# Kernel tuning notes

Hardware: AMD Instinct MI355X
Metric: run time of the kernel (lower is better)

## Reference

```python
import jax, jax.numpy as jnp
import numpy as np

D = 1024
H = 16
HD = D // H
FFN = D * 2
EPS = 1e-5


def _layernorm(x, g, b):
    mu = jnp.mean(x, axis=-1, keepdims=True)
    var = jnp.var(x, axis=-1, keepdims=True)
    return (x - mu) * jax.lax.rsqrt(var + EPS) * g + b


def setup_inputs() -> dict:
    key = jax.random.key(0)
    ks = jax.random.split(key, 12)
    s = 1.0 / np.sqrt(D)
    inp = {
        "x": jax.random.normal(ks[0], (2, 2048, D), dtype=jnp.float32),
        "Wq": jax.random.normal(ks[1], (D, D), dtype=jnp.float32) * s,
        "bq": jnp.zeros((D,), jnp.float32),
        "Wk": jax.random.normal(ks[2], (D, D), dtype=jnp.float32) * s,
        "bk": jnp.zeros((D,), jnp.float32),
        "Wv": jax.random.normal(ks[3], (D, D), dtype=jnp.float32) * s,
        "bv": jnp.zeros((D,), jnp.float32),
        "Wo": jax.random.normal(ks[4], (D, D), dtype=jnp.float32) * s,
        "bo": jnp.zeros((D,), jnp.float32),
        "g1": jnp.ones((D,), jnp.float32),
        "b1": jnp.zeros((D,), jnp.float32),
        "W_ff1": jax.random.normal(ks[5], (D, FFN), dtype=jnp.float32) * s,
        "b_ff1": jnp.zeros((FFN,), jnp.float32),
        "W_ff2": jax.random.normal(ks[6], (FFN, D), dtype=jnp.float32) * (1.0 / np.sqrt(FFN)),
        "b_ff2": jnp.zeros((D,), jnp.float32),
        "g2": jnp.ones((D,), jnp.float32),
        "b2": jnp.zeros((D,), jnp.float32),
    }
    return inp


def reference(x, Wq, bq, Wk, bk, Wv, bv, Wo, bo, g1, b1, W_ff1, b_ff1, W_ff2, b_ff2, g2, b2):
    B, S, _ = x.shape
    # QKV projections -> [B, H, S, HD]
    def split_heads(t):
        return t.reshape(B, S, H, HD).transpose(0, 2, 1, 3)
    Q = split_heads(x @ Wq + bq)
    K = split_heads(x @ Wk + bk)
    V = split_heads(x @ Wv + bv)
    scores = jnp.einsum('bhqd,bhkd->bhqk', Q, K) / np.sqrt(HD).astype(np.float32)
    attn = jax.nn.softmax(scores, axis=-1)  # dropout = identity in eval
    ctx = jnp.einsum('bhqk,bhkd->bhqd', attn, V)
    ctx = ctx.transpose(0, 2, 1, 3).reshape(B, S, D)
    x = _layernorm(x + ctx @ Wo + bo, g1, b1)
    h = jax.nn.gelu(x @ W_ff1 + b_ff1, approximate=False)
    x = _layernorm(x + h @ W_ff2 + b_ff2, g2, b2)
    return x
```

## Files before the change

kernel.cpp:

```cpp
#include <hip/hip_runtime.h>

#define SEQ 2048
#define NTOK 4096
#define DM 1024
#define LDQK 3072

typedef __attribute__((ext_vector_type(4))) float f32x4;
typedef __attribute__((ext_vector_type(8))) short short8;
typedef __attribute__((ext_vector_type(4))) short short4v;

__device__ __forceinline__ short f2bf(float f) {
  union { float f; unsigned u; } x; x.f = f;
  unsigned r = x.u + 0x7fffu + ((x.u >> 16) & 1u);
  return (short)(r >> 16);
}

__device__ __forceinline__ float bf2f(short s) {
  union { unsigned u; float f; } x;
  x.u = ((unsigned)(unsigned short)s) << 16;
  return x.f;
}

__device__ __forceinline__ void async_load16(const void* g, void* l) {
  __builtin_amdgcn_global_load_lds(
      (const __attribute__((address_space(1))) void*)g,
      (__attribute__((address_space(3))) void*)l, 16, 0, 0);
}

__global__ void __launch_bounds__(256) prep_all(
    const float* __restrict__ Wq, const float* __restrict__ Wk,
    const float* __restrict__ Wv, const float* __restrict__ Wo,
    const float* __restrict__ Wf1, const float* __restrict__ Wf2,
    const float* __restrict__ x,
    short* __restrict__ Wqkv, short* __restrict__ Wto,
    short* __restrict__ Wtf1, short* __restrict__ Wtf2,
    short* __restrict__ xb) {
  const int z = blockIdx.z;
  const int tx = threadIdx.x, ty = threadIdx.y;
  if (z == 6) {
    int blk = blockIdx.y * 64 + blockIdx.x;
    int i = blk * 256 + ty * 32 + tx;
    f32x4 v = ((const f32x4*)x)[i];
    short4v o;
#pragma unroll
    for (int j = 0; j < 4; ++j) o[j] = f2bf(v[j]);
    ((short4v*)xb)[i] = o;
    return;
  }
  const float* in;
  short* out;
  int K, N;
  switch (z) {
    case 0: in = Wq;  out = Wqkv;               K = 1024; N = 1024; break;
    case 1: in = Wk;  out = Wqkv + 1024 * 1024; K = 1024; N = 1024; break;
    case 2: in = Wv;  out = Wqkv + 2048 * 1024; K = 1024; N = 1024; break;
    case 3: in = Wo;  out = Wto;                K = 1024; N = 1024; break;
    case 4: in = Wf1; out = Wtf1;               K = 1024; N = 2048; break;
    default: in = Wf2; out = Wtf2;              K = 2048; N = 1024; break;
  }
  if (blockIdx.x * 32 >= N || blockIdx.y * 32 >= K) return;
  __shared__ float t[32][33];
  const int n = blockIdx.x * 32 + tx;
#pragma unroll
  for (int i = 0; i < 4; ++i) {
    int k = blockIdx.y * 32 + ty + i * 8;
    t[ty + i * 8][tx] = in[(size_t)k * N + n];
  }
  __syncthreads();
  const int k2 = blockIdx.y * 32 + tx;
#pragma unroll
  for (int i = 0; i < 4; ++i) {
    int n2 = blockIdx.x * 32 + ty + i * 8;
    out[(size_t)n2 * K + k2] = f2bf(t[tx][ty + i * 8]);
  }
}

__global__ void __launch_bounds__(512, 2) gemm_qkv8(
    const short* __restrict__ A, const short* __restrict__ Bt,
    const float* __restrict__ bq, const float* __restrict__ bk,
    const float* __restrict__ bv, short* __restrict__ Cout,
    short* __restrict__ VtOut) {
  __shared__ __align__(16) short As[128 * 64];
  __shared__ __align__(16) short Bs[256 * 64];
  const int tid = threadIdx.x;
  const int w = tid >> 6, lane = tid & 63;
  const int hi = lane >> 4, lo = lane & 15;
  const int bx = blockIdx.x, bm = blockIdx.y;
  const int wr = w >> 2, wc = w & 3;
  f32x4 acc[4][4] = {};

  for (int kt = 0; kt < 16; ++kt) {
#pragma unroll
    for (int i = 0; i < 2; ++i) {
      int c = i * 512 + tid;
      int r = c >> 3, scc = (c & 7) ^ (r & 7);
      async_load16(A + (size_t)(bm * 128 + r) * 1024 + kt * 64 + scc * 8,
                   &As[(i * 8 + w) * 512]);
    }
#pragma unroll
    for (int i = 0; i < 4; ++i) {
      int c = i * 512 + tid;
      int r = c >> 3, scc = (c & 7) ^ (r & 7);
      async_load16(Bt + (size_t)(bx * 256 + r) * 1024 + kt * 64 + scc * 8,
                   &Bs[(i * 8 + w) * 512]);
    }
    __syncthreads();
#pragma unroll
    for (int ks = 0; ks < 2; ++ks) {
      short8 af[4], bf[4];
#pragma unroll
      for (int m = 0; m < 4; ++m) {
        int row = wr * 64 + m * 16 + lo;
        int ch = (ks * 4 + hi) ^ (row & 7);
        af[m] = *(const short8*)(&As[row * 64 + ch * 8]);
      }
#pragma unroll
      for (int n = 0; n < 4; ++n) {
        int row = wc * 64 + n * 16 + lo;
        int ch = (ks * 4 + hi) ^ (row & 7);
        bf[n] = *(const short8*)(&Bs[row * 64 + ch * 8]);
      }
#pragma unroll
      for (int m = 0; m < 4; ++m)
#pragma unroll
        for (int n = 0; n < 4; ++n)
          acc[m][n] = __builtin_amdgcn_mfma_f32_16x16x32_bf16(af[m], bf[n], acc[m][n], 0, 0, 0);
    }
    __syncthreads();
  }
  const int colb = bx * 256 + wc * 64 + lo;
#pragma unroll
  for (int m = 0; m < 4; ++m) {
    int row0 = bm * 128 + wr * 64 + m * 16 + hi * 4;
#pragma unroll
    for (int n = 0; n < 4; ++n) {
      int col = colb + n * 16;
      int r3 = col >> 10;
      const float* bp = (r3 == 0) ? bq : ((r3 == 1) ? bk : bv);
      float bs = bp[col & 1023];
      if (r3 == 2) {
        int vdim = col - 2048;
        int hh = vdim >> 6, dd = vdim & 63;
        int bb = row0 >> 11, ss = row0 & 2047;
        short4v t;
#pragma unroll
        for (int j = 0; j < 4; ++j) t[j] = f2bf(acc[m][n][j] + bs);
        *(short4v*)&VtOut[((size_t)(bb * 16 + hh) * 64 + dd) * SEQ + ss] = t;
      } else {
#pragma unroll
        for (int j = 0; j < 4; ++j)
          Cout[(size_t)(row0 + j) * LDQK + col] = f2bf(acc[m][n][j] + bs);
      }
    }
  }
}

template <int EPI, bool DBUF>
__global__ void __launch_bounds__(256, 2) gemm_bt(
    const short* __restrict__ A, const short* __restrict__ Bt,
    const float* __restrict__ b0, void* __restrict__ Cout,
    int M, int N, int K) {
  __shared__ __align__(16) short As[DBUF ? 2 * 128 * 64 : 128 * 64];
  __shared__ __align__(16) short Bs[DBUF ? 2 * 128 * 64 : 128 * 64];
  const int w = threadIdx.x >> 6, lane = threadIdx.x & 63;
  const int hi = lane >> 4, lo = lane & 15;
  const int bm = blockIdx.y, bn = blockIdx.x;
  const int wr = w >> 1, wc = w & 1;
  f32x4 acc[4][4] = {};
  const int nkt = K >> 6;

  auto stage = [&](int kt, int buf) {
#pragma unroll
    for (int j = 0; j < 4; ++j) {
      int c = (j * 4 + w) * 64 + lane;
      int r = c >> 3;
      int scc = (c & 7) ^ (r & 7);
      async_load16(A + (size_t)(bm * 128 + r) * K + kt * 64 + scc * 8,
                   &As[buf * (128 * 64) + (j * 4 + w) * 512]);
      async_load16(Bt + (size_t)(bn * 128 + r) * K + kt * 64 + scc * 8,
                   &Bs[buf * (128 * 64) + (j * 4 + w) * 512]);
    }
  };

  if (DBUF) {
    stage(0, 0);
    __syncthreads();
  }

  for (int kt = 0; kt < nkt; ++kt) {
    int buf = 0;
    if (DBUF) {
      buf = kt & 1;
      if (kt + 1 < nkt) stage(kt + 1, buf ^ 1);
    } else {
      stage(kt, 0);
      __syncthreads();
    }
#pragma unroll
    for (int ks = 0; ks < 2; ++ks) {
      short8 af[4], bf[4];
#pragma unroll
      for (int m = 0; m < 4; ++m) {
        int row = wr * 64 + m * 16 + lo;
        int ch = (ks * 4 + hi) ^ (row & 7);
        af[m] = *(const short8*)(&As[buf * (128 * 64) + row * 64 + ch * 8]);
      }
#pragma unroll
      for (int n = 0; n < 4; ++n) {
        int row = wc * 64 + n * 16 + lo;
        int ch = (ks * 4 + hi) ^ (row & 7);
        bf[n] = *(const short8*)(&Bs[buf * (128 * 64) + row * 64 + ch * 8]);
      }
#pragma unroll
      for (int m = 0; m < 4; ++m)
#pragma unroll
        for (int n = 0; n < 4; ++n)
          acc[m][n] = __builtin_amdgcn_mfma_f32_16x16x32_bf16(af[m], bf[n], acc[m][n], 0, 0, 0);
    }
    __syncthreads();
  }
  const int colb = bn * 128 + wc * 64 + lo;
#pragma unroll
  for (int m = 0; m < 4; ++m) {
    int row0 = bm * 128 + wr * 64 + m * 16 + hi * 4;
#pragma unroll
    for (int n = 0; n < 4; ++n) {
      int col = colb + n * 16;
      float bs = b0[col];
#pragma unroll
      for (int j = 0; j < 4; ++j) {
        float v = acc[m][n][j] + bs;
        if (EPI == 1) v = 0.5f * v * (1.f + erff(v * 0.70710678f));
        ((short*)Cout)[(size_t)(row0 + j) * N + col] = f2bf(v);
      }
    }
  }
}

__global__ void __launch_bounds__(256, 2) gemm_n64(
    const short* __restrict__ A, const short* __restrict__ Bt,
    const float* __restrict__ b0, const short* __restrict__ resid,
    short* __restrict__ Cout, int M, int N, int K) {
  __shared__ __align__(16) short As[2][128 * 64];
  __shared__ __align__(16) short Bs[2][64 * 64];
  const int w = threadIdx.x >> 6, lane = threadIdx.x & 63;
  const int hi = lane >> 4, lo = lane & 15;
  const int bm = blockIdx.y, bn = blockIdx.x;
  const int wr = w >> 1, wc = w & 1;
  f32x4 acc[4][2] = {};
  const int nkt = K >> 6;

  auto stage = [&](int kt, int buf) {
#pragma unroll
    for (int j = 0; j < 4; ++j) {
      int c = (j * 4 + w) * 64 + lane;
      int r = c >> 3;
      int scc = (c & 7) ^ (r & 7);
      async_load16(A + (size_t)(bm * 128 + r) * K + kt * 64 + scc * 8,
                   &As[buf][(j * 4 + w) * 512]);
    }
#pragma unroll
    for (int j = 0; j < 2; ++j) {
      int c = j * 256 + w * 64 + lane;
      int r = c >> 3;
      int scc = (c & 7) ^ (r & 7);
      async_load16(Bt + (size_t)(bn * 64 + r) * K + kt * 64 + scc * 8,
                   &Bs[buf][(j * 256 + w * 64) * 8]);
    }
  };

  stage(0, 0);
  __syncthreads();

  for (int kt = 0; kt < nkt; ++kt) {
    const int buf = kt & 1;
    if (kt + 1 < nkt) stage(kt + 1, buf ^ 1);
#pragma unroll
    for (int ks = 0; ks < 2; ++ks) {
      short8 af[4], bf[2];
#pragma unroll
      for (int m = 0; m < 4; ++m) {
        int row = wr * 64 + m * 16 + lo;
        int ch = (ks * 4 + hi) ^ (row & 7);
        af[m] = *(const short8*)(&As[buf][row * 64 + ch * 8]);
      }
#pragma unroll
      for (int n = 0; n < 2; ++n) {
        int row = wc * 32 + n * 16 + lo;
        int ch = (ks * 4 + hi) ^ (row & 7);
        bf[n] = *(const short8*)(&Bs[buf][row * 64 + ch * 8]);
      }
#pragma unroll
      for (int m = 0; m < 4; ++m)
#pragma unroll
        for (int n = 0; n < 2; ++n)
          acc[m][n] = __builtin_amdgcn_mfma_f32_16x16x32_bf16(af[m], bf[n], acc[m][n], 0, 0, 0);
    }
    __syncthreads();
  }
  const int colb = bn * 64 + wc * 32 + lo;
#pragma unroll
  for (int m = 0; m < 4; ++m) {
    int row0 = bm * 128 + wr * 64 + m * 16 + hi * 4;
#pragma unroll
    for (int n = 0; n < 2; ++n) {
      int col = colb + n * 16;
      float bs = b0[col];
#pragma unroll
      for (int j = 0; j < 4; ++j) {
        size_t idx = (size_t)(row0 + j) * N + col;
        Cout[idx] = f2bf(acc[m][n][j] + bs + bf2f(resid[idx]));
      }
    }
  }
}

__global__ void __launch_bounds__(256, 2) attn_kernel(
    const short* __restrict__ Qb, const short* __restrict__ Kb,
    const short* __restrict__ Vt, short* __restrict__ ctx) {
  const int w = threadIdx.x >> 6, lane = threadIdx.x & 63;
  const int hi = lane >> 4, lo = lane & 15;
  const int tid = threadIdx.x;
  const int L = blockIdx.x;
  const int W = (L & 7) * 128 + (L >> 3);
  const int qt = W & 31, bh = W >> 5;
  const int b = bh >> 4, h = bh & 15;
  const int qbase = qt * 64 + w * 16;
  const float C = 0.18033688f;

  __shared__ __align__(16) short Ks[2][64 * 64];
  __shared__ __align__(16) short Vs[2][64 * 64];
  __shared__ __align__(16) short P[4][16 * 64];

  const short* qp = Qb + (size_t)(b * SEQ + qbase + lo) * LDQK + h * 64;
  short8 bq[2];
#pragma unroll
  for (int c = 0; c < 2; ++c)
    bq[c] = *(const short8*)(qp + c * 32 + hi * 8);

  const short* kb = Kb + (size_t)(b * SEQ) * LDQK + h * 64;
  const short* vb = Vt + (size_t)bh * 64 * SEQ;

  auto stage = [&](int kt, int buf) {
    const short* kg = kb + (size_t)(kt * 64) * LDQK;
#pragma unroll
    for (int i = 0; i < 2; ++i) {
      int c = i * 256 + tid;
      int r = c >> 3, scc = (c & 7) ^ (r & 7);
      async_load16(kg + (size_t)r * LDQK + scc * 8,
                   &Ks[buf][(i * 256 + w * 64) * 8]);
    }
    const short* vg = vb + kt * 64;
#pragma unroll
    for (int i = 0; i < 2; ++i) {
      int c = i * 256 + tid;
      int r = c >> 3, sc2 = (c & 7) ^ (r & 7);
      async_load16(vg + (size_t)r * SEQ + sc2 * 8,
                   &Vs[buf][(i * 256 + w * 64) * 8]);
    }
  };

  stage(0, 0);
  __syncthreads();

  f32x4 o[4] = {};
  float lacc = 0.f;
  const int x7 = lo & 7;

  for (int kt = 0; kt < SEQ / 64; ++kt) {
    const int buf = kt & 1;
    if (kt + 1 < SEQ / 64) stage(kt + 1, buf ^ 1);

    f32x4 s[4] = {};
    __builtin_amdgcn_s_setprio(1);
#pragma unroll
    for (int g = 0; g < 4; ++g) {
      const short* kr = &Ks[buf][(g * 16 + lo) * 64];
      short8 ka0 = *(const short8*)(kr + ((hi) ^ x7) * 8);
      short8 ka1 = *(const short8*)(kr + ((4 + hi) ^ x7) * 8);
      s[g] = __builtin_amdgcn_mfma_f32_16x16x32_bf16(ka0, bq[0], s[g], 0, 0, 0);
      s[g] = __builtin_amdgcn_mfma_f32_16x16x32_bf16(ka1, bq[1], s[g], 0, 0, 0);
    }
    __builtin_amdgcn_s_setprio(0);
    short8 vv[2][4];
#pragma unroll
    for (int ks = 0; ks < 2; ++ks)
#pragma unroll
      for (int a = 0; a < 4; ++a)
        vv[ks][a] = *(const short8*)(&Vs[buf][(a * 16 + lo) * 64 + (((ks * 4 + hi) ^ x7) * 8)]);

    float rsg[4];
    short* pbase = &P[w][0];
#pragma unroll
    for (int g = 0; g < 4; ++g) {
      float p0 = exp2f(s[g][0] * C);
      float p1 = exp2f(s[g][1] * C);
      float p2 = exp2f(s[g][2] * C);
      float p3 = exp2f(s[g][3] * C);
      rsg[g] = (p0 + p1) + (p2 + p3);
      unsigned w0, w1;
      asm("v_cvt_pk_bf16_f32 %0, %1, %2" : "=v"(w0) : "v"(p0), "v"(p1));
      asm("v_cvt_pk_bf16_f32 %0, %1, %2" : "=v"(w1) : "v"(p2), "v"(p3));
      union { unsigned uu[2]; short4v s4; } cv;
      cv.uu[0] = w0; cv.uu[1] = w1;
      int pc = (2 * g + (hi >> 1)) ^ x7;
      *(short4v*)(pbase + lo * 64 + pc * 8 + (hi & 1) * 4) = cv.s4;
    }
    __builtin_amdgcn_s_setprio(1);
#pragma unroll
    for (int ks = 0; ks < 2; ++ks) {
      int pc = (ks * 4 + hi) ^ x7;
      short8 pa = *(const short8*)(pbase + lo * 64 + pc * 8);
#pragma unroll
      for (int a = 0; a < 4; ++a)
        o[a] = __builtin_amdgcn_mfma_f32_16x16x32_bf16(pa, vv[ks][a], o[a], 0, 0, 0);
    }
    __builtin_amdgcn_s_setprio(0);
    lacc += (rsg[0] + rsg[1]) + (rsg[2] + rsg[3]);
    __syncthreads();
  }
  lacc += __shfl_xor(lacc, 16);
  lacc += __shfl_xor(lacc, 32);
#pragma unroll
  for (int j = 0; j < 4; ++j) {
    float lj = __shfl(lacc, hi * 4 + j);
    float inv = 1.f / lj;
    int row = qbase + hi * 4 + j;
#pragma unroll
    for (int a = 0; a < 4; ++a)
      ctx[(size_t)(b * SEQ + row) * DM + h * 64 + a * 16 + lo] = f2bf(o[a][j] * inv);
  }
}

__global__ void __launch_bounds__(256) ln_bf16(
    const short* __restrict__ in, const float* __restrict__ g,
    const float* __restrict__ beta, float* __restrict__ outf,
    short* __restrict__ outb) {
  const int row = blockIdx.x;
  const int t = threadIdx.x;
  const size_t base = (size_t)row * DM;
  short4v iv = ((const short4v*)(in + base))[t];
  f32x4 v;
#pragma unroll
  for (int j = 0; j < 4; ++j) v[j] = bf2f(iv[j]);
  float s = v[0] + v[1] + v[2] + v[3];
  float s2 = v[0] * v[0] + v[1] * v[1] + v[2] * v[2] + v[3] * v[3];
#pragma unroll
  for (int off = 1; off < 64; off <<= 1) {
    s += __shfl_xor(s, off);
    s2 += __shfl_xor(s2, off);
  }
  __shared__ float rs[4], rs2[4];
  if ((t & 63) == 0) { rs[t >> 6] = s; rs2[t >> 6] = s2; }
  __syncthreads();
  s = rs[0] + rs[1] + rs[2] + rs[3];
  s2 = rs2[0] + rs2[1] + rs2[2] + rs2[3];
  float mu = s * (1.f / DM);
  float var = s2 * (1.f / DM) - mu * mu;
  float rstd = rsqrtf(var + 1e-5f);
  f32x4 gv = ((const f32x4*)g)[t];
  f32x4 bv = ((const f32x4*)beta)[t];
  f32x4 ov;
#pragma unroll
  for (int j = 0; j < 4; ++j) ov[j] = (v[j] - mu) * rstd * gv[j] + bv[j];
  if (outf) ((f32x4*)(outf + base))[t] = ov;
  if (outb) {
    short4v sb;
#pragma unroll
    for (int j = 0; j < 4; ++j) sb[j] = f2bf(ov[j]);
    ((short4v*)(outb + base))[t] = sb;
  }
}

extern "C" void kernel_launch(void* const* d_in, const int* in_sizes, int n_in,
                              void* d_out, int out_size, void* d_ws, size_t ws_size,
                              hipStream_t stream) {
  (void)in_sizes; (void)n_in; (void)out_size; (void)ws_size;
  const float* x   = (const float*)d_in[0];
  const float* Wq  = (const float*)d_in[1];
  const float* bq  = (const float*)d_in[2];
  const float* Wk  = (const float*)d_in[3];
  const float* bk  = (const float*)d_in[4];
  const float* Wv  = (const float*)d_in[5];
  const float* bv  = (const float*)d_in[6];
  const float* Wo  = (const float*)d_in[7];
  const float* bo  = (const float*)d_in[8];
  const float* g1  = (const float*)d_in[9];
  const float* b1  = (const float*)d_in[10];
  const float* Wf1 = (const float*)d_in[11];
  const float* bf1 = (const float*)d_in[12];
  const float* Wf2 = (const float*)d_in[13];
  const float* bf2 = (const float*)d_in[14];
  const float* g2  = (const float*)d_in[15];
  const float* b2  = (const float*)d_in[16];

  char* ws = (char*)d_ws;
  const size_t MB = 1u << 20;
  short* Wqkv = (short*)(ws + 0 * MB);
  short* Wto  = (short*)(ws + 6 * MB);
  short* Wtf1 = (short*)(ws + 8 * MB);
  short* Wtf2 = (short*)(ws + 12 * MB);
  short* xb   = (short*)(ws + 16 * MB);
  short* QKV  = (short*)(ws + 24 * MB);
  short* Vt   = (short*)(ws + 48 * MB);
  short* ctxb = (short*)(ws + 56 * MB);
  short* aout = (short*)(ws + 64 * MB);
  short* x1b  = (short*)(ws + 72 * MB);
  short* hb   = QKV;
  short* ffo  = (short*)(ws + 48 * MB);

  prep_all<<<dim3(64, 64, 7), dim3(32, 8), 0, stream>>>(
      Wq, Wk, Wv, Wo, Wf1, Wf2, x, Wqkv, Wto, Wtf1, Wtf2, xb);

  gemm_qkv8<<<dim3(12, 32), 512, 0, stream>>>(xb, Wqkv, bq, bk, bv, QKV, Vt);

  attn_kernel<<<dim3(1024), 256, 0, stream>>>(QKV, QKV + 1024, Vt, ctxb);

  gemm_n64<<<dim3(16, 32), 256, 0, stream>>>(ctxb, Wto, bo, xb, aout, NTOK, 1024, 1024);
  ln_bf16<<<4096, 256, 0, stream>>>(aout, g1, b1, nullptr, x1b);
  gemm_bt<1, true><<<dim3(16, 32), 256, 0, stream>>>(
      x1b, Wtf1, bf1, hb, NTOK, 2048, 1024);
  gemm_n64<<<dim3(16, 32), 256, 0, stream>>>(hb, Wtf2, bf2, x1b, ffo, NTOK, 1024, 2048);
  ln_bf16<<<4096, 256, 0, stream>>>(ffo, g2, b2, (float*)d_out, nullptr);
}
```

Before: 206.5 us.

## Replace output-proj and FFN GEMMs with unified 8-wave single-buffered kernel

Swaps the double-buffered 4-wave gemm_bt and gemm_n64 kernels for one templated 512-thread, 8-wave kernel used by the output projection and both FFN GEMMs. It uses larger N tiles (128 or 256) with a single LDS buffer. The aim is more waves per CU to hide latency and more reuse per tile, with fewer blocks (256 instead of 512). The cost is that loads no longer overlap compute, since each k-step stages synchronously, and the larger per-block tile may reduce occupancy.

Measured after the change: 217.1 us. 5.1% more time.

```diff
diff --git a/kernel.cpp b/kernel.cpp
--- a/kernel.cpp
+++ b/kernel.cpp
@@ -155,161 +155,76 @@
   }
 }
 
-template <int EPI, bool DBUF>
-__global__ void __launch_bounds__(256, 2) gemm_bt(
+template <int EPI, int BN, bool RESID>
+__global__ void __launch_bounds__(512, 2) gemm_w8(
     const short* __restrict__ A, const short* __restrict__ Bt,
-    const float* __restrict__ b0, void* __restrict__ Cout,
-    int M, int N, int K) {
-  __shared__ __align__(16) short As[DBUF ? 2 * 128 * 64 : 128 * 64];
-  __shared__ __align__(16) short Bs[DBUF ? 2 * 128 * 64 : 128 * 64];
-  const int w = threadIdx.x >> 6, lane = threadIdx.x & 63;
+    const float* __restrict__ b0, const short* __restrict__ resid,
+    short* __restrict__ Cout, int M, int N, int K) {
+  constexpr int FR = BN / 64;
+  __shared__ __align__(16) short As[128 * 64];
+  __shared__ __align__(16) short Bs[BN * 64];
+  const int tid = threadIdx.x;
+  const int w = tid >> 6, lane = tid & 63;
   const int hi = lane >> 4, lo = lane & 15;
-  const int bm = blockIdx.y, bn = blockIdx.x;
-  const int wr = w >> 1, wc = w & 1;
-  f32x4 acc[4][4] = {};
+  const int bx = blockIdx.x, bm = blockIdx.y;
+  const int wr = w >> 2, wc = w & 3;
+  f32x4 acc[4][FR] = {};
   const int nkt = K >> 6;
 
-  auto stage = [&](int kt, int buf) {
-#pragma unroll
-    for (int j = 0; j < 4; ++j) {
-      int c = (j * 4 + w) * 64 + lane;
-      int r = c >> 3;
-      int scc = (c & 7) ^ (r & 7);
+  for (int kt = 0; kt < nkt; ++kt) {
+#pragma unroll
+    for (int i = 0; i < 2; ++i) {
+      int c = i * 512 + tid;
+      int r = c >> 3, scc = (c & 7) ^ (r & 7);
       async_load16(A + (size_t)(bm * 128 + r) * K + kt * 64 + scc * 8,
-                   &As[buf * (128 * 64) + (j * 4 + w) * 512]);
-      async_load16(Bt + (size_t)(bn * 128 + r) * K + kt * 64 + scc * 8,
-                   &Bs[buf * (128 * 64) + (j * 4 + w) * 512]);
-    }
-  };
-
-  if (DBUF) {
-    stage(0, 0);
+                   &As[(i * 8 + w) * 512]);
+    }
+#pragma unroll
+    for (int i = 0; i < BN / 64; ++i) {
+      int c = i * 512 + tid;
+      int r = c >> 3, scc = (c & 7) ^ (r & 7);
+      async_load16(Bt + (size_t)(bx * BN + r) * K + kt * 64 + scc * 8,
+                   &Bs[(i * 8 + w) * 512]);
+    }
     __syncthreads();
-  }
-
-  for (int kt = 0; kt < nkt; ++kt) {
-    int buf = 0;
-    if (DBUF) {
-      buf = kt & 1;
-      if (kt + 1 < nkt) stage(kt + 1, buf ^ 1);
-    } else {
-      stage(kt, 0);
-      __syncthreads();
-    }
 #pragma unroll
     for (int ks = 0; ks < 2; ++ks) {
-      short8 af[4], bf[4];
+      short8 af[4], bf[FR];
 #pragma unroll
       for (int m = 0; m < 4; ++m) {
         int row = wr * 64 + m * 16 + lo;
         int ch = (ks * 4 + hi) ^ (row & 7);
-        af[m] = *(const short8*)(&As[buf * (128 * 64) + row * 64 + ch * 8]);
-      }
-#pragma unroll
-      for (int n = 0; n < 4; ++n) {
-        int row = wc * 64 + n * 16 + lo;
+        af[m] = *(const short8*)(&As[row * 64 + ch * 8]);
+      }
+#pragma unroll
+      for (int n = 0; n < FR; ++n) {
+        int row = wc * (BN / 4) + n * 16 + lo;
         int ch = (ks * 4 + hi) ^ (row & 7);
-        bf[n] = *(const short8*)(&Bs[buf * (128 * 64) + row * 64 + ch * 8]);
+        bf[n] = *(const short8*)(&Bs[row * 64 + ch * 8]);
       }
 #pragma unroll
       for (int m = 0; m < 4; ++m)
 #pragma unroll
-        for (int n = 0; n < 4; ++n)
+        for (int n = 0; n < FR; ++n)
           acc[m][n] = __builtin_amdgcn_mfma_f32_16x16x32_bf16(af[m], bf[n], acc[m][n], 0, 0, 0);
     }
     __syncthreads();
   }
-  const int colb = bn * 128 + wc * 64 + lo;
+  const int colb = bx * BN + wc * (BN / 4) + lo;
 #pragma unroll
   for (int m = 0; m < 4; ++m) {
     int row0 = bm * 128 + wr * 64 + m * 16 + hi * 4;
 #pragma unroll
-    for (int n = 0; n < 4; ++n) {
+    for (int n = 0; n < FR; ++n) {
       int col = colb + n * 16;
       float bs = b0[col];
 #pragma unroll
       for (int j = 0; j < 4; ++j) {
+        size_t idx = (size_t)(row0 + j) * N + col;
         float v = acc[m][n][j] + bs;
         if (EPI == 1) v = 0.5f * v * (1.f + erff(v * 0.70710678f));
-        ((short*)Cout)[(size_t)(row0 + j) * N + col] = f2bf(v);
-      }
-    }
-  }
-}
-
-__global__ void __launch_bounds__(256, 2) gemm_n64(
-    const short* __restrict__ A, const short* __restrict__ Bt,
-    const float* __restrict__ b0, const short* __restrict__ resid,
-    short* __restrict__ Cout, int M, int N, int K) {
-  __shared__ __align__(16) short As[2][128 * 64];
-  __shared__ __align__(16) short Bs[2][64 * 64];
-  const int w = threadIdx.x >> 6, lane = threadIdx.x & 63;
-  const int hi = lane >> 4, lo = lane & 15;
-  const int bm = blockIdx.y, bn = blockIdx.x;
-  const int wr = w >> 1, wc = w & 1;
-  f32x4 acc[4][2] = {};
-  const int nkt = K >> 6;
-
-  auto stage = [&](int kt, int buf) {
-#pragma unroll
-    for (int j = 0; j < 4; ++j) {
-      int c = (j * 4 + w) * 64 + lane;
-      int r = c >> 3;
-      int scc = (c & 7) ^ (r & 7);
-      async_load16(A + (size_t)(bm * 128 + r) * K + kt * 64 + scc * 8,
-                   &As[buf][(j * 4 + w) * 512]);
-    }
-#pragma unroll
-    for (int j = 0; j < 2; ++j) {
-      int c = j * 256 + w * 64 + lane;
-      int r = c >> 3;
-      int scc = (c & 7) ^ (r & 7);
-      async_load16(Bt + (size_t)(bn * 64 + r) * K + kt * 64 + scc * 8,
-                   &Bs[buf][(j * 256 + w * 64) * 8]);
-    }
-  };
-
-  stage(0, 0);
-  __syncthreads();
-
-  for (int kt = 0; kt < nkt; ++kt) {
-    const int buf = kt & 1;
-    if (kt + 1 < nkt) stage(kt + 1, buf ^ 1);
-#pragma unroll
-    for (int ks = 0; ks < 2; ++ks) {
-      short8 af[4], bf[2];
-#pragma unroll
-      for (int m = 0; m < 4; ++m) {
-        int row = wr * 64 + m * 16 + lo;
-        int ch = (ks * 4 + hi) ^ (row & 7);
-        af[m] = *(const short8*)(&As[buf][row * 64 + ch * 8]);
-      }
-#pragma unroll
-      for (int n = 0; n < 2; ++n) {
-        int row = wc * 32 + n * 16 + lo;
-        int ch = (ks * 4 + hi) ^ (row & 7);
-        bf[n] = *(const short8*)(&Bs[buf][row * 64 + ch * 8]);
-      }
-#pragma unroll
-      for (int m = 0; m < 4; ++m)
-#pragma unroll
-        for (int n = 0; n < 2; ++n)
-          acc[m][n] = __builtin_amdgcn_mfma_f32_16x16x32_bf16(af[m], bf[n], acc[m][n], 0, 0, 0);
-    }
-    __syncthreads();
-  }
-  const int colb = bn * 64 + wc * 32 + lo;
-#pragma unroll
-  for (int m = 0; m < 4; ++m) {
-    int row0 = bm * 128 + wr * 64 + m * 16 + hi * 4;
-#pragma unroll
-    for (int n = 0; n < 2; ++n) {
-      int col = colb + n * 16;
-      float bs = b0[col];
-#pragma unroll
-      for (int j = 0; j < 4; ++j) {
-        size_t idx = (size_t)(row0 + j) * N + col;
-        Cout[idx] = f2bf(acc[m][n][j] + bs + bf2f(resid[idx]));
+        if (RESID) v += bf2f(resid[idx]);
+        Cout[idx] = f2bf(v);
       }
     }
   }
@@ -516,10 +431,12 @@
 
   attn_kernel<<<dim3(1024), 256, 0, stream>>>(QKV, QKV + 1024, Vt, ctxb);
 
-  gemm_n64<<<dim3(16, 32), 256, 0, stream>>>(ctxb, Wto, bo, xb, aout, NTOK, 1024, 1024);
+  gemm_w8<0, 128, true><<<dim3(8, 32), 512, 0, stream>>>(
+      ctxb, Wto, bo, xb, aout, NTOK, 1024, 1024);
   ln_bf16<<<4096, 256, 0, stream>>>(aout, g1, b1, nullptr, x1b);
-  gemm_bt<1, true><<<dim3(16, 32), 256, 0, stream>>>(
-      x1b, Wtf1, bf1, hb, NTOK, 2048, 1024);
-  gemm_n64<<<dim3(16, 32), 256, 0, stream>>>(hb, Wtf2, bf2, x1b, ffo, NTOK, 1024, 2048);
+  gemm_w8<1, 256, false><<<dim3(8, 32), 512, 0, stream>>>(
+      x1b, Wtf1, bf1, nullptr, hb, NTOK, 2048, 1024);
+  gemm_w8<0, 128, true><<<dim3(8, 32), 512, 0, stream>>>(
+      hb, Wtf2, bf2, x1b, ffo, NTOK, 1024, 2048);
   ln_bf16<<<4096, 256, 0, stream>>>(ffo, g2, b2, (float*)d_out, nullptr);
 }
```
